# Kernel tuning notes

Hardware: AMD Instinct MI355X
Metric: run time of the kernel (lower is better)

Reference implementation:

```python
import jax, jax.numpy as jnp
import numpy as np

ALPHA = 0.3
TEMPERATURE = 2.0
LN_EPS = 1e-5
NORM_EPS = 1e-8


def setup_inputs() -> dict:
    key = jax.random.key(0)
    k1, k2 = jax.random.split(key)
    B, N, D = 2, 4096, 512
    F = D // 2 + 1  # rfft output bins = 257
    x = jax.random.normal(k1, (B, N, D), dtype=jnp.float32)
    # spectral_proj: Linear(F, F, bias=False); kaiming-uniform-ish scale
    W_spec = jax.random.normal(k2, (F, F), dtype=jnp.float32) * (1.0 / np.sqrt(F))
    gamma = jnp.ones((D,), dtype=jnp.float32)   # LayerNorm weight
    beta = jnp.zeros((D,), dtype=jnp.float32)   # LayerNorm bias
    return {"x": x, "W_spec": W_spec, "gamma": gamma, "beta": beta}


def reference(x, W_spec, gamma, beta):
    # x: (B, N, D) real
    x_hat = jnp.fft.rfft(x, axis=-1)                       # (B, N, F) complex64
    # complex input through real-weight linear: x_hat @ W^T
    x_hat = jnp.einsum('bnf,gf->bng', x_hat, W_spec.astype(x_hat.dtype))
    # complex magnitude normalization per token
    norms = jnp.sqrt(jnp.sum(jnp.abs(x_hat) ** 2, axis=-1, keepdims=True) + NORM_EPS)
    x_norm = x_hat / norms                                 # (B, N, F) complex
    # spectral correlation: |x_norm @ x_norm^H|
    S = jnp.abs(jnp.einsum('bnf,bmf->bnm', x_norm, jnp.conj(x_norm)))  # (B, N, N) real
    S_soft = jax.nn.softmax(S / TEMPERATURE, axis=-1)      # dropout is identity (eval)
    mixed = jnp.einsum('bnm,bmd->bnd', S_soft, x)          # (B, N, D)
    h = x + ALPHA * (mixed - x)                            # residual blend
    # LayerNorm over last dim
    mu = jnp.mean(h, axis=-1, keepdims=True)
    var = jnp.mean((h - mu) ** 2, axis=-1, keepdims=True)
    out = (h - mu) / jnp.sqrt(var + LN_EPS) * gamma + beta
    return out, S
```

## Files before the change

### kernel.cpp

```cpp
#include <hip/hip_runtime.h>
#include <hip/hip_bf16.h>
#include <math.h>

#define BB 2
#define NN 4096
#define DD 512
#define FF 257
#define FP 288
#define KK2 (2*FP)
#define NT 528
#define PI_F 3.14159265358979323846f

typedef __attribute__((ext_vector_type(4))) float f32x4;
typedef __attribute__((ext_vector_type(8))) short bf16x8;
typedef unsigned int u32;
typedef unsigned short u16;

#define MT_OFF  0u
#define XF_OFF  1052672u
#define SS_OFF  10489856u
#define NR_OFF  (SS_OFF + 8388608u)
#define XT_OFF  77598720u
#define MX_OFF  85987328u

#define AS1 __attribute__((address_space(1)))
#define AS3 __attribute__((address_space(3)))

static __device__ __forceinline__ void gl2lds(const u16* g, u16* l) {
    __builtin_amdgcn_global_load_lds((const AS1 u32*)(unsigned long long)g,
                                     (AS3 u32*)(unsigned)(unsigned long long)l,
                                     16, 0, 0);
}

static __device__ __forceinline__ unsigned short f2bf(float f) {
    unsigned int u = __float_as_uint(f);
    unsigned int r = (u + 0x7fffu + ((u >> 16) & 1u)) >> 16;
    return (unsigned short)r;
}
static __device__ __forceinline__ float bf2f(unsigned short s) {
    return __uint_as_float(((unsigned int)s) << 16);
}

static __device__ __forceinline__ bf16x8 conj_swap(bf16x8 a) {
    union { bf16x8 v; u32 u[4]; } s, d;
    s.v = a;
#pragma unroll
    for (int i = 0; i < 4; ++i) {
        u32 w = s.u[i];
        d.u[i] = ((w >> 16) | (w << 16)) ^ 0x80000000u;
    }
    return d.v;
}

__global__ __launch_bounds__(256) void k_zero(float* __restrict__ norms,
                                              u16* __restrict__ Mt) {
    int i = blockIdx.x * 256 + threadIdx.x;
    if (i < 8192) norms[i] = 0.f;
    Mt[514 * 512 + i] = 0;
}

__global__ __launch_bounds__(512) void k_build_Mt(const float* __restrict__ W,
                                                  u16* __restrict__ Mt) {
    __shared__ float twr[512], twi[512], wrow[FF];
    const int g = blockIdx.x;
    const int d = threadIdx.x;
    {
        float s, c;
        sincosf(-(2.0f * PI_F / 512.0f) * (float)d, &s, &c);
        twr[d] = c; twi[d] = s;
    }
    for (int f = d; f < FF; f += 512) wrow[f] = W[g * FF + f];
    __syncthreads();
    float re = 0.f, im = 0.f;
    for (int f = 0; f < FF; ++f) {
        float w = wrow[f];
        int k = (f * d) & 511;
        re = fmaf(w, twr[k], re);
        im = fmaf(w, twi[k], im);
    }
    Mt[(size_t)(2 * g) * 512 + d]     = f2bf(re);
    Mt[(size_t)(2 * g + 1) * 512 + d] = f2bf(im);
}

__global__ __launch_bounds__(256) void k_xcast(const float* __restrict__ x,
                                               u16* __restrict__ xb) {
    const size_t i = ((size_t)blockIdx.x * 256 + threadIdx.x) * 8;
    float4 a = *(const float4*)(x + i);
    float4 b = *(const float4*)(x + i + 4);
    union { u16 h[8]; uint4 q; } o;
    o.h[0] = f2bf(a.x); o.h[1] = f2bf(a.y); o.h[2] = f2bf(a.z); o.h[3] = f2bf(a.w);
    o.h[4] = f2bf(b.x); o.h[5] = f2bf(b.y); o.h[6] = f2bf(b.z); o.h[7] = f2bf(b.w);
    *(uint4*)(xb + i) = o.q;
}

__global__ __launch_bounds__(256) void k_proj_mfma(const u16* __restrict__ xb,
                                                   const u16* __restrict__ Mt,
                                                   u16* __restrict__ xhat,
                                                   float* __restrict__ norms) {
    __shared__ u16 As[128 * 64];
    __shared__ u16 Bs[64 * 64];
    const int prow = blockIdx.y * 128;
    const int gcol = blockIdx.x * 64;
    const int tid = threadIdx.x;
    const int lane = tid & 63;
    const int wave = tid >> 6;
    const int wr = wave * 32;
    const int fr = lane & 15;
    const int q  = lane >> 4;
    const int sw = lane & 7;

    const u16* __restrict__ Arow = xb + (size_t)prow * DD;
    const u16* __restrict__ Brow = Mt + (size_t)gcol * DD;

    const int cs0 = (q ^ sw) * 8;
    const int cs1 = ((4 + q) ^ sw) * 8;

    f32x4 acc[2][4];
#pragma unroll
    for (int m = 0; m < 2; ++m)
#pragma unroll
        for (int n = 0; n < 4; ++n) acc[m][n] = (f32x4)0.f;

    int rA[2], rB[4];
#pragma unroll
    for (int m = 0; m < 2; ++m) rA[m] = (wr + m * 16 + fr) * 64;
#pragma unroll
    for (int n = 0; n < 4; ++n) rB[n] = (n * 16 + fr) * 64;

    for (int kc = 0; kc < DD / 64; ++kc) {
        const int k0 = kc * 64;
        __syncthreads();
#pragma unroll
        for (int it = 0; it < 4; ++it) {
            int e = tid + it * 256;
            int row = e >> 3, ch = e & 7;
            gl2lds(Arow + (size_t)row * DD + k0 + (ch ^ (row & 7)) * 8, &As[e * 8]);
        }
#pragma unroll
        for (int it = 0; it < 2; ++it) {
            int e = tid + it * 256;
            int row = e >> 3, ch = e & 7;
            gl2lds(Brow + (size_t)row * DD + k0 + (ch ^ (row & 7)) * 8, &Bs[e * 8]);
        }
        __syncthreads();
#pragma unroll
        for (int kk = 0; kk < 2; ++kk) {
            const int cs = kk ? cs1 : cs0;
            bf16x8 av[2], bv[4];
#pragma unroll
            for (int m = 0; m < 2; ++m) av[m] = *(const bf16x8*)&As[rA[m] + cs];
#pragma unroll
            for (int n = 0; n < 4; ++n) bv[n] = *(const bf16x8*)&Bs[rB[n] + cs];
#pragma unroll
            for (int m = 0; m < 2; ++m)
#pragma unroll
                for (int n = 0; n < 4; ++n)
                    acc[m][n] = __builtin_amdgcn_mfma_f32_16x16x32_bf16(av[m], bv[n], acc[m][n], 0, 0, 0);
        }
    }

#pragma unroll
    for (int m = 0; m < 2; ++m) {
#pragma unroll
        for (int reg = 0; reg < 4; ++reg) {
            const int r = prow + wr + m * 16 + q * 4 + reg;
            u16* __restrict__ rp = xhat + (size_t)r * KK2 + gcol + fr;
            float sq = 0.f;
#pragma unroll
            for (int n = 0; n < 4; ++n) {
                float v = acc[m][n][reg];
                rp[n * 16] = f2bf(v);
                sq = fmaf(v, v, sq);
            }
            sq += __shfl_xor(sq, 1);
            sq += __shfl_xor(sq, 2);
            sq += __shfl_xor(sq, 4);
            sq += __shfl_xor(sq, 8);
            if (fr == 0) atomicAdd(&norms[r], sq);
        }
    }
}

__global__ __launch_bounds__(256) void k_normalize(u32* __restrict__ Xf,
                                                   const float* __restrict__ norms) {
    const int row = blockIdx.x * 8 + (threadIdx.x >> 5);
    const int l = threadIdx.x & 31;
    const float rn = rsqrtf(norms[row] + 1e-8f);
    u32* __restrict__ p = Xf + (size_t)row * FP;
#pragma unroll
    for (int u = 0; u < 9; ++u) {
        u32 w = p[u * 32 + l];
        float lo = bf2f((u16)(w & 0xffffu)) * rn;
        float hi = bf2f((u16)(w >> 16)) * rn;
        p[u * 32 + l] = (u32)f2bf(lo) | ((u32)f2bf(hi) << 16);
    }
}

__global__ __launch_bounds__(256) void k_gram_mfma(const u16* __restrict__ Xf,
                                                   float* __restrict__ Sout) {
    __shared__ u16 Af[128 * 64];
    __shared__ u16 Bf[128 * 64];
    __shared__ float trs[32][129];
    int i = (int)blockIdx.x;
    int b = 0;
    if (i >= NT) { b = 1; i -= NT; }
    int a = 0;
    while (i >= 32 - a) { i -= 32 - a; ++a; }
    const int brow = a * 128;
    const int bcol = (a + i) * 128;

    const int tid = threadIdx.x;
    const int lane = tid & 63;
    const int wave = tid >> 6;
    const int wr = (wave >> 1) * 64;
    const int wc = (wave & 1) * 64;
    const int fr = lane & 15;
    const int q  = lane >> 4;
    const int sw = lane & 7;

    const u16* __restrict__ Arow = Xf + (size_t)(b * NN + brow) * KK2;
    const u16* __restrict__ Brow = Xf + (size_t)(b * NN + bcol) * KK2;

    int srow[4], soff[4];
#pragma unroll
    for (int it = 0; it < 4; ++it) {
        int e = tid + it * 256;
        int row = e >> 3, ch = e & 7;
        srow[it] = row;
        soff[it] = (ch ^ (row & 7)) * 8;
    }
    const int cs0 = (q ^ sw) * 8;
    const int cs1 = ((4 + q) ^ sw) * 8;

    f32x4 acc_re[4][4], acc_im[4][4];
#pragma unroll
    for (int m = 0; m < 4; ++m)
#pragma unroll
        for (int n = 0; n < 4; ++n) {
            acc_re[m][n] = (f32x4)0.f;
            acc_im[m][n] = (f32x4)0.f;
        }

    int rA[4], rB[4];
#pragma unroll
    for (int m = 0; m < 4; ++m) rA[m] = (wr + m * 16 + fr) * 64;
#pragma unroll
    for (int n = 0; n < 4; ++n) rB[n] = (wc + n * 16 + fr) * 64;

    for (int kc = 0; kc < KK2 / 64; ++kc) {
        const int k0 = kc * 64;
        __syncthreads();
#pragma unroll
        for (int it = 0; it < 4; ++it) {
            int e = tid + it * 256;
            gl2lds(Arow + (size_t)srow[it] * KK2 + k0 + soff[it], &Af[e * 8]);
            gl2lds(Brow + (size_t)srow[it] * KK2 + k0 + soff[it], &Bf[e * 8]);
        }
        __syncthreads();
#pragma unroll
        for (int kk = 0; kk < 2; ++kk) {
            const int cs = kk ? cs1 : cs0;
            bf16x8 av[4], bv[4], gv[4];
#pragma unroll
            for (int m = 0; m < 4; ++m) av[m] = *(const bf16x8*)&Af[rA[m] + cs];
#pragma unroll
            for (int n = 0; n < 4; ++n) bv[n] = *(const bf16x8*)&Bf[rB[n] + cs];
#pragma unroll
            for (int m = 0; m < 4; ++m) gv[m] = conj_swap(av[m]);
#pragma unroll
            for (int m = 0; m < 4; ++m)
#pragma unroll
                for (int n = 0; n < 4; ++n) {
                    acc_re[m][n] = __builtin_amdgcn_mfma_f32_16x16x32_bf16(av[m], bv[n], acc_re[m][n], 0, 0, 0);
                    acc_im[m][n] = __builtin_amdgcn_mfma_f32_16x16x32_bf16(gv[m], bv[n], acc_im[m][n], 0, 0, 0);
                }
        }
    }

    float* __restrict__ Sb = Sout + (size_t)b * NN * NN;
#pragma unroll
    for (int m = 0; m < 4; ++m) {
#pragma unroll
        for (int reg = 0; reg < 4; ++reg) {
            int r = brow + wr + m * 16 + q * 4 + reg;
            float* __restrict__ rp = Sb + (size_t)r * NN + bcol + wc + fr;
#pragma unroll
            for (int n = 0; n < 4; ++n) {
                float re = acc_re[m][n][reg], im = acc_im[m][n][reg];
                rp[n * 16] = sqrtf(fmaf(re, re, im * im));
            }
        }
    }
    if (brow == bcol) return;

#pragma unroll
    for (int p = 0; p < 4; ++p) {
        __syncthreads();
        if ((wave >> 1) == (p >> 1)) {
            const int mbase = (p & 1) * 2;
#pragma unroll
            for (int mm = 0; mm < 2; ++mm) {
                const int m = mbase + mm;
                const int i0 = mm * 16 + q * 4;
#pragma unroll
                for (int reg = 0; reg < 4; ++reg) {
#pragma unroll
                    for (int n = 0; n < 4; ++n) {
                        float re = acc_re[m][n][reg], im = acc_im[m][n][reg];
                        trs[i0 + reg][wc + n * 16 + fr] = sqrtf(fmaf(re, re, im * im));
                    }
                }
            }
        }
        __syncthreads();
        const int j0 = (tid & 7) * 4;
#pragma unroll
        for (int u = 0; u < 4; ++u) {
            const int mr = u * 32 + (tid >> 3);
            float4 v;
            v.x = trs[j0 + 0][mr];
            v.y = trs[j0 + 1][mr];
            v.z = trs[j0 + 2][mr];
            v.w = trs[j0 + 3][mr];
            *(float4*)(Sb + (size_t)(bcol + mr) * NN + brow + p * 32 + j0) = v;
        }
    }
}

__global__ __launch_bounds__(256) void k_softmax(const float* __restrict__ S,
                                                 unsigned short* __restrict__ Wout) {
    __shared__ float red[8];
    const size_t row = blockIdx.x;
    const int tid = threadIdx.x;
    const float4* __restrict__ p4 = (const float4*)(S + row * NN);
    float4 v[4];
    float vmax = -1e30f;
#pragma unroll
    for (int u = 0; u < 4; ++u) {
        v[u] = p4[u * 256 + tid];
        vmax = fmaxf(vmax, fmaxf(fmaxf(v[u].x, v[u].y), fmaxf(v[u].z, v[u].w)));
    }
    for (int off = 32; off > 0; off >>= 1) vmax = fmaxf(vmax, __shfl_down(vmax, off, 64));
    if ((tid & 63) == 0) red[tid >> 6] = vmax;
    __syncthreads();
    const float bmax = fmaxf(fmaxf(red[0], red[1]), fmaxf(red[2], red[3]));
    float s = 0.f;
#pragma unroll
    for (int u = 0; u < 4; ++u) {
        v[u].x = __expf((v[u].x - bmax) * 0.5f);
        v[u].y = __expf((v[u].y - bmax) * 0.5f);
        v[u].z = __expf((v[u].z - bmax) * 0.5f);
        v[u].w = __expf((v[u].w - bmax) * 0.5f);
        s += (v[u].x + v[u].y) + (v[u].z + v[u].w);
    }
    for (int off = 32; off > 0; off >>= 1) s += __shfl_down(s, off, 64);
    if ((tid & 63) == 0) red[4 + (tid >> 6)] = s;
    __syncthreads();
    const float rinv = 1.0f / ((red[4] + red[5]) + (red[6] + red[7]));
    ushort4* __restrict__ o4 = (ushort4*)(Wout + row * NN);
#pragma unroll
    for (int u = 0; u < 4; ++u) {
        ushort4 w;
        w.x = f2bf(v[u].x * rinv);
        w.y = f2bf(v[u].y * rinv);
        w.z = f2bf(v[u].z * rinv);
        w.w = f2bf(v[u].w * rinv);
        o4[u * 256 + tid] = w;
    }
}

__global__ __launch_bounds__(256) void k_xpose(const float* __restrict__ x,
                                               u16* __restrict__ xbT) {
    __shared__ u16 st[64][72];
    const int b = blockIdx.z;
    const int t0 = blockIdx.x * 64;
    const int d0 = blockIdx.y * 64;
    const int tid = threadIdx.x;
#pragma unroll
    for (int u = 0; u < 4; ++u) {
        int idx = tid + u * 256;
        int tl = idx >> 4, d4 = (idx & 15) * 4;
        float4 v = *(const float4*)(x + ((size_t)(b * NN) + t0 + tl) * DD + d0 + d4);
        st[tl][d4 + 0] = f2bf(v.x);
        st[tl][d4 + 1] = f2bf(v.y);
        st[tl][d4 + 2] = f2bf(v.z);
        st[tl][d4 + 3] = f2bf(v.w);
    }
    __syncthreads();
#pragma unroll
    for (int u = 0; u < 2; ++u) {
        int e = tid + u * 256;
        int dl = e >> 3, t8 = (e & 7) * 8;
        union { u16 h[8]; uint4 q; } o;
#pragma unroll
        for (int j = 0; j < 8; ++j) o.h[j] = st[t8 + j][dl];
        *(uint4*)(xbT + ((size_t)(b * DD) + d0 + dl) * NN + t0 + t8) = o.q;
    }
}

__global__ __launch_bounds__(256) void k_mixed_mfma(const u16* __restrict__ Ws,
                                                    const u16* __restrict__ xbT,
                                                    float* __restrict__ mixed) {
    __shared__ u16 As[64 * 64];
    __shared__ u16 Bs[128 * 64];
    const int b = blockIdx.z;
    const int brow = blockIdx.y * 64;
    const int bcol = blockIdx.x * 128;
    const int tid = threadIdx.x;
    const int lane = tid & 63;
    const int wave = tid >> 6;
    const int wr = (wave >> 1) * 32;
    const int wc = (wave & 1) * 64;
    const int fr = lane & 15;
    const int q  = lane >> 4;
    const int sw = lane & 7;

    const u16* __restrict__ Arow = Ws + (size_t)(b * NN + brow) * NN;
    const u16* __restrict__ Brow = xbT + ((size_t)(b * DD) + bcol) * NN;

    const int cs0 = (q ^ sw) * 8;
    const int cs1 = ((4 + q) ^ sw) * 8;

    f32x4 acc[2][4];
#pragma unroll
    for (int m = 0; m < 2; ++m)
#pragma unroll
        for (int n = 0; n < 4; ++n) acc[m][n] = (f32x4)0.f;

    int rA[2], rB[4];
#pragma unroll
    for (int m = 0; m < 2; ++m) rA[m] = (wr + m * 16 + fr) * 64;
#pragma unroll
    for (int n = 0; n < 4; ++n) rB[n] = (wc + n * 16 + fr) * 64;

    for (int kc = 0; kc < NN / 64; ++kc) {
        const int k0 = kc * 64;
        __syncthreads();
#pragma unroll
        for (int it = 0; it < 2; ++it) {
            int e = tid + it * 256;
            int row = e >> 3, ch = e & 7;
            gl2lds(Arow + (size_t)row * NN + k0 + (ch ^ (row & 7)) * 8, &As[e * 8]);
        }
#pragma unroll
        for (int it = 0; it < 4; ++it) {
            int e = tid + it * 256;
            int row = e >> 3, ch = e & 7;
            gl2lds(Brow + (size_t)row * NN + k0 + (ch ^ (row & 7)) * 8, &Bs[e * 8]);
        }
        __syncthreads();
#pragma unroll
        for (int kk = 0; kk < 2; ++kk) {
            const int cs = kk ? cs1 : cs0;
            bf16x8 av[2], bv[4];
#pragma unroll
            for (int m = 0; m < 2; ++m) av[m] = *(const bf16x8*)&As[rA[m] + cs];
#pragma unroll
            for (int n = 0; n < 4; ++n) bv[n] = *(const bf16x8*)&Bs[rB[n] + cs];
#pragma unroll
            for (int m = 0; m < 2; ++m)
#pragma unroll
                for (int n = 0; n < 4; ++n)
                    acc[m][n] = __builtin_amdgcn_mfma_f32_16x16x32_bf16(av[m], bv[n], acc[m][n], 0, 0, 0);
        }
    }

    float* __restrict__ ob = mixed + (size_t)b * NN * DD;
#pragma unroll
    for (int m = 0; m < 2; ++m) {
#pragma unroll
        for (int reg = 0; reg < 4; ++reg) {
            int r = brow + wr + m * 16 + q * 4 + reg;
            float* __restrict__ rp = ob + (size_t)r * DD + bcol + wc + fr;
#pragma unroll
            for (int n = 0; n < 4; ++n) rp[n * 16] = acc[m][n][reg];
        }
    }
}

__global__ __launch_bounds__(256) void k_ln(const float* __restrict__ x,
                                            const float* __restrict__ mixed,
                                            const float* __restrict__ gamma,
                                            const float* __restrict__ beta,
                                            float* __restrict__ out) {
    __shared__ float red[8];
    const size_t row = blockIdx.x;
    const int tid = threadIdx.x;
    const float* __restrict__ xr = x + row * DD;
    const float* __restrict__ mr = mixed + row * DD;
    float x0 = xr[tid], x1 = xr[tid + 256];
    float h0 = fmaf(0.3f, mr[tid] - x0, x0);
    float h1 = fmaf(0.3f, mr[tid + 256] - x1, x1);
    float s = h0 + h1;
    float sq = fmaf(h0, h0, h1 * h1);
    for (int off = 32; off > 0; off >>= 1) {
        s += __shfl_down(s, off, 64);
        sq += __shfl_down(sq, off, 64);
    }
    if ((tid & 63) == 0) { red[tid >> 6] = s; red[4 + (tid >> 6)] = sq; }
    __syncthreads();
    const float mu = ((red[0] + red[1]) + (red[2] + red[3])) * (1.0f / DD);
    const float var = ((red[4] + red[5]) + (red[6] + red[7])) * (1.0f / DD) - mu * mu;
    const float rstd = rsqrtf(var + 1e-5f);
    out[row * DD + tid] = fmaf((h0 - mu) * rstd, gamma[tid], beta[tid]);
    out[row * DD + tid + 256] = fmaf((h1 - mu) * rstd, gamma[tid + 256], beta[tid + 256]);
}

extern "C" void kernel_launch(void* const* d_in, const int* in_sizes, int n_in,
                              void* d_out, int out_size, void* d_ws, size_t ws_size,
                              hipStream_t stream) {
    const float* x     = (const float*)d_in[0];
    const float* Wspec = (const float*)d_in[1];
    const float* gamma = (const float*)d_in[2];
    const float* beta  = (const float*)d_in[3];
    float* out  = (float*)d_out;
    float* Sout = out + (size_t)BB * NN * DD;

    char* ws = (char*)d_ws;
    u16*   Mt    = (u16*)(ws + MT_OFF);
    u16*   Xf    = (u16*)(ws + XF_OFF);
    u32*   XfW   = (u32*)(ws + XF_OFF);
    u16*   xb    = (u16*)(ws + SS_OFF);
    float* norms = (float*)(ws + NR_OFF);
    u16*   Ssoft = (u16*)(ws + SS_OFF);
    u16*   xbT   = (u16*)(ws + XT_OFF);
    float* mixed = (float*)(ws + MX_OFF);

    hipLaunchKernelGGL(k_zero, dim3(124), dim3(256), 0, stream, norms, Mt);
    hipLaunchKernelGGL(k_build_Mt, dim3(257), dim3(512), 0, stream, Wspec, Mt);
    hipLaunchKernelGGL(k_xcast, dim3(2048), dim3(256), 0, stream, x, xb);
    hipLaunchKernelGGL(k_proj_mfma, dim3(KK2 / 64, (BB * NN) / 128), dim3(256), 0, stream,
                       xb, Mt, Xf, norms);
    hipLaunchKernelGGL(k_normalize, dim3(BB * NN / 8), dim3(256), 0, stream, XfW, norms);
    hipLaunchKernelGGL(k_gram_mfma, dim3(BB * NT), dim3(256), 0, stream, Xf, Sout);
    hipLaunchKernelGGL(k_softmax, dim3(BB * NN), dim3(256), 0, stream, Sout, Ssoft);
    hipLaunchKernelGGL(k_xpose, dim3(NN / 64, DD / 64, BB), dim3(256), 0, stream, x, xbT);
    hipLaunchKernelGGL(k_mixed_mfma, dim3(DD / 128, NN / 64, BB), dim3(256), 0, stream, Ssoft, xbT, mixed);
    hipLaunchKernelGGL(k_ln, dim3(BB * NN), dim3(256), 0, stream, x, mixed, gamma, beta, out);
}
```

Before: 386.5 us.

## Fuse softmax into gram epilogue and mixing GEMM, fuse LayerNorm into mixing

Drops the separate softmax kernel. The gram kernel's epilogue now accumulates per-row exp sums, with no max subtraction because |S| <= 1, using atomics into a new lsum buffer. The mixing GEMM reads fp32 S directly, exponentiates and casts to bf16 while staging A tiles, then applies normalization, the residual blend and LayerNorm in its epilogue. This removes the bf16 softmax round trip, the mixed buffer and two launches. In exchange the mixing kernel re-reads fp32 S (twice the bytes of bf16), repeats exp work, holds a much larger LDS B tile (64 KB) with 32-row tiles that lower occupancy, and the gram kernel gains atomics.

```diff
diff --git a/kernel.cpp b/kernel.cpp
--- a/kernel.cpp
+++ b/kernel.cpp
@@ -10,6 +10,7 @@
 #define KK2 (2*FP)
 #define NT 528
 #define PI_F 3.14159265358979323846f
+#define CEXP 0.72134752044f
 
 typedef __attribute__((ext_vector_type(4))) float f32x4;
 typedef __attribute__((ext_vector_type(8))) short bf16x8;
@@ -18,10 +19,10 @@
 
 #define MT_OFF  0u
 #define XF_OFF  1052672u
-#define SS_OFF  10489856u
-#define NR_OFF  (SS_OFF + 8388608u)
+#define XB_OFF  10489856u
+#define NR_OFF  (XB_OFF + 8388608u)
+#define L_OFF   (NR_OFF + 32768u)
 #define XT_OFF  77598720u
-#define MX_OFF  85987328u
 
 #define AS1 __attribute__((address_space(1)))
 #define AS3 __attribute__((address_space(3)))
@@ -53,9 +54,10 @@
 }
 
 __global__ __launch_bounds__(256) void k_zero(float* __restrict__ norms,
+                                              float* __restrict__ l,
                                               u16* __restrict__ Mt) {
     int i = blockIdx.x * 256 + threadIdx.x;
-    if (i < 8192) norms[i] = 0.f;
+    if (i < 8192) { norms[i] = 0.f; l[i] = 0.f; }
     Mt[514 * 512 + i] = 0;
 }
 
@@ -197,10 +199,13 @@
 }
 
 __global__ __launch_bounds__(256) void k_gram_mfma(const u16* __restrict__ Xf,
-                                                   float* __restrict__ Sout) {
-    __shared__ u16 Af[128 * 64];
-    __shared__ u16 Bf[128 * 64];
-    __shared__ float trs[32][129];
+                                                   float* __restrict__ Sout,
+                                                   float* __restrict__ lsum) {
+    __shared__ __align__(16) char gsm[32768];
+    u16* Af = (u16*)gsm;
+    u16* Bf = (u16*)(gsm + 16384);
+    float (*trs)[129] = (float (*)[129])gsm;
+
     int i = (int)blockIdx.x;
     int b = 0;
     if (i >= NT) { b = 1; i -= NT; }
@@ -278,17 +283,26 @@
     }
 
     float* __restrict__ Sb = Sout + (size_t)b * NN * NN;
+    float* __restrict__ lb = lsum + (size_t)b * NN;
 #pragma unroll
     for (int m = 0; m < 4; ++m) {
 #pragma unroll
         for (int reg = 0; reg < 4; ++reg) {
             int r = brow + wr + m * 16 + q * 4 + reg;
             float* __restrict__ rp = Sb + (size_t)r * NN + bcol + wc + fr;
+            float psum = 0.f;
 #pragma unroll
             for (int n = 0; n < 4; ++n) {
                 float re = acc_re[m][n][reg], im = acc_im[m][n][reg];
-                rp[n * 16] = sqrtf(fmaf(re, re, im * im));
+                float s = sqrtf(fmaf(re, re, im * im));
+                rp[n * 16] = s;
+                psum += exp2f(s * CEXP);
             }
+            psum += __shfl_xor(psum, 1);
+            psum += __shfl_xor(psum, 2);
+            psum += __shfl_xor(psum, 4);
+            psum += __shfl_xor(psum, 8);
+            if (fr == 0) atomicAdd(&lb[r], psum);
         }
     }
     if (brow == bcol) return;
@@ -323,49 +337,13 @@
             v.z = trs[j0 + 2][mr];
             v.w = trs[j0 + 3][mr];
             *(float4*)(Sb + (size_t)(bcol + mr) * NN + brow + p * 32 + j0) = v;
-        }
-    }
-}
-
-__global__ __launch_bounds__(256) void k_softmax(const float* __restrict__ S,
-                                                 unsigned short* __restrict__ Wout) {
-    __shared__ float red[8];
-    const size_t row = blockIdx.x;
-    const int tid = threadIdx.x;
-    const float4* __restrict__ p4 = (const float4*)(S + row * NN);
-    float4 v[4];
-    float vmax = -1e30f;
-#pragma unroll
-    for (int u = 0; u < 4; ++u) {
-        v[u] = p4[u * 256 + tid];
-        vmax = fmaxf(vmax, fmaxf(fmaxf(v[u].x, v[u].y), fmaxf(v[u].z, v[u].w)));
-    }
-    for (int off = 32; off > 0; off >>= 1) vmax = fmaxf(vmax, __shfl_down(vmax, off, 64));
-    if ((tid & 63) == 0) red[tid >> 6] = vmax;
-    __syncthreads();
-    const float bmax = fmaxf(fmaxf(red[0], red[1]), fmaxf(red[2], red[3]));
-    float s = 0.f;
-#pragma unroll
-    for (int u = 0; u < 4; ++u) {
-        v[u].x = __expf((v[u].x - bmax) * 0.5f);
-        v[u].y = __expf((v[u].y - bmax) * 0.5f);
-        v[u].z = __expf((v[u].z - bmax) * 0.5f);
-        v[u].w = __expf((v[u].w - bmax) * 0.5f);
-        s += (v[u].x + v[u].y) + (v[u].z + v[u].w);
-    }
-    for (int off = 32; off > 0; off >>= 1) s += __shfl_down(s, off, 64);
-    if ((tid & 63) == 0) red[4 + (tid >> 6)] = s;
-    __syncthreads();
-    const float rinv = 1.0f / ((red[4] + red[5]) + (red[6] + red[7]));
-    ushort4* __restrict__ o4 = (ushort4*)(Wout + row * NN);
-#pragma unroll
-    for (int u = 0; u < 4; ++u) {
-        ushort4 w;
-        w.x = f2bf(v[u].x * rinv);
-        w.y = f2bf(v[u].y * rinv);
-        w.z = f2bf(v[u].z * rinv);
-        w.w = f2bf(v[u].w * rinv);
-        o4[u * 256 + tid] = w;
+            float ps = exp2f(v.x * CEXP) + exp2f(v.y * CEXP)
+                     + exp2f(v.z * CEXP) + exp2f(v.w * CEXP);
+            ps += __shfl_xor(ps, 1);
+            ps += __shfl_xor(ps, 2);
+            ps += __shfl_xor(ps, 4);
+            if ((tid & 7) == 0) atomicAdd(&lb[bcol + mr], ps);
+        }
     }
 }
 
@@ -398,112 +376,132 @@
     }
 }
 
-__global__ __launch_bounds__(256) void k_mixed_mfma(const u16* __restrict__ Ws,
-                                                    const u16* __restrict__ xbT,
-                                                    float* __restrict__ mixed) {
-    __shared__ u16 As[64 * 64];
-    __shared__ u16 Bs[128 * 64];
-    const int b = blockIdx.z;
-    const int brow = blockIdx.y * 64;
-    const int bcol = blockIdx.x * 128;
+__global__ __launch_bounds__(256) void k_mixed_fused(const float* __restrict__ S,
+                                                     const float* __restrict__ lsum,
+                                                     const u16* __restrict__ xbT,
+                                                     const float* __restrict__ x,
+                                                     const float* __restrict__ gamma,
+                                                     const float* __restrict__ beta,
+                                                     float* __restrict__ out) {
+    __shared__ __align__(16) u16 Bs[DD * 64];
+    __shared__ __align__(16) u16 As[32 * 64];
+    __shared__ float red[32][8];
+    const int b = blockIdx.y;
+    const int t0 = blockIdx.x * 32;
     const int tid = threadIdx.x;
     const int lane = tid & 63;
     const int wave = tid >> 6;
-    const int wr = (wave >> 1) * 32;
-    const int wc = (wave & 1) * 64;
     const int fr = lane & 15;
     const int q  = lane >> 4;
     const int sw = lane & 7;
-
-    const u16* __restrict__ Arow = Ws + (size_t)(b * NN + brow) * NN;
-    const u16* __restrict__ Brow = xbT + ((size_t)(b * DD) + bcol) * NN;
+    const int dcol = wave * 128;
+
+    const float* __restrict__ Srow = S + ((size_t)b * NN + t0) * NN;
+    const u16* __restrict__ Brow = xbT + (size_t)b * DD * NN;
 
     const int cs0 = (q ^ sw) * 8;
     const int cs1 = ((4 + q) ^ sw) * 8;
 
-    f32x4 acc[2][4];
+    const int ar = tid >> 3;
+    const int ach = tid & 7;
+    const float* __restrict__ aSrc = Srow + (size_t)ar * NN + ach * 8;
+    u16* __restrict__ aDst = As + ar * 64 + (ach ^ (ar & 7)) * 8;
+
+    f32x4 acc[2][8];
 #pragma unroll
     for (int m = 0; m < 2; ++m)
 #pragma unroll
-        for (int n = 0; n < 4; ++n) acc[m][n] = (f32x4)0.f;
-
-    int rA[2], rB[4];
-#pragma unroll
-    for (int m = 0; m < 2; ++m) rA[m] = (wr + m * 16 + fr) * 64;
-#pragma unroll
-    for (int n = 0; n < 4; ++n) rB[n] = (wc + n * 16 + fr) * 64;
+        for (int n = 0; n < 8; ++n) acc[m][n] = (f32x4)0.f;
+
+    int rA[2], rB[8];
+#pragma unroll
+    for (int m = 0; m < 2; ++m) rA[m] = (m * 16 + fr) * 64;
+#pragma unroll
+    for (int n = 0; n < 8; ++n) rB[n] = (dcol + n * 16 + fr) * 64;
 
     for (int kc = 0; kc < NN / 64; ++kc) {
         const int k0 = kc * 64;
         __syncthreads();
 #pragma unroll
-        for (int it = 0; it < 2; ++it) {
-            int e = tid + it * 256;
-            int row = e >> 3, ch = e & 7;
-            gl2lds(Arow + (size_t)row * NN + k0 + (ch ^ (row & 7)) * 8, &As[e * 8]);
-        }
-#pragma unroll
-        for (int it = 0; it < 4; ++it) {
+        for (int it = 0; it < 16; ++it) {
             int e = tid + it * 256;
             int row = e >> 3, ch = e & 7;
             gl2lds(Brow + (size_t)row * NN + k0 + (ch ^ (row & 7)) * 8, &Bs[e * 8]);
         }
+        {
+            float4 a0 = *(const float4*)(aSrc + k0);
+            float4 a1 = *(const float4*)(aSrc + k0 + 4);
+            union { u16 h[8]; uint4 v; } pk;
+            pk.h[0] = f2bf(exp2f(a0.x * CEXP));
+            pk.h[1] = f2bf(exp2f(a0.y * CEXP));
+            pk.h[2] = f2bf(exp2f(a0.z * CEXP));
+            pk.h[3] = f2bf(exp2f(a0.w * CEXP));
+            pk.h[4] = f2bf(exp2f(a1.x * CEXP));
+            pk.h[5] = f2bf(exp2f(a1.y * CEXP));
+            pk.h[6] = f2bf(exp2f(a1.z * CEXP));
+            pk.h[7] = f2bf(exp2f(a1.w * CEXP));
+            *(uint4*)aDst = pk.v;
+        }
         __syncthreads();
 #pragma unroll
         for (int kk = 0; kk < 2; ++kk) {
             const int cs = kk ? cs1 : cs0;
-            bf16x8 av[2], bv[4];
+            bf16x8 av[2], bv[8];
 #pragma unroll
             for (int m = 0; m < 2; ++m) av[m] = *(const bf16x8*)&As[rA[m] + cs];
 #pragma unroll
-            for (int n = 0; n < 4; ++n) bv[n] = *(const bf16x8*)&Bs[rB[n] + cs];
+            for (int n = 0; n < 8; ++n) bv[n] = *(const bf16x8*)&Bs[rB[n] + cs];
 #pragma unroll
             for (int m = 0; m < 2; ++m)
 #pragma unroll
-                for (int n = 0; n < 4; ++n)
+                for (int n = 0; n < 8; ++n)
                     acc[m][n] = __builtin_amdgcn_mfma_f32_16x16x32_bf16(av[m], bv[n], acc[m][n], 0, 0, 0);
         }
     }
 
-    float* __restrict__ ob = mixed + (size_t)b * NN * DD;
+    __syncthreads();
 #pragma unroll
     for (int m = 0; m < 2; ++m) {
 #pragma unroll
         for (int reg = 0; reg < 4; ++reg) {
-            int r = brow + wr + m * 16 + q * 4 + reg;
-            float* __restrict__ rp = ob + (size_t)r * DD + bcol + wc + fr;
-#pragma unroll
-            for (int n = 0; n < 4; ++n) rp[n * 16] = acc[m][n][reg];
-        }
-    }
-}
-
-__global__ __launch_bounds__(256) void k_ln(const float* __restrict__ x,
-                                            const float* __restrict__ mixed,
-                                            const float* __restrict__ gamma,
-                                            const float* __restrict__ beta,
-                                            float* __restrict__ out) {
-    __shared__ float red[8];
-    const size_t row = blockIdx.x;
-    const int tid = threadIdx.x;
-    const float* __restrict__ xr = x + row * DD;
-    const float* __restrict__ mr = mixed + row * DD;
-    float x0 = xr[tid], x1 = xr[tid + 256];
-    float h0 = fmaf(0.3f, mr[tid] - x0, x0);
-    float h1 = fmaf(0.3f, mr[tid + 256] - x1, x1);
-    float s = h0 + h1;
-    float sq = fmaf(h0, h0, h1 * h1);
-    for (int off = 32; off > 0; off >>= 1) {
-        s += __shfl_down(s, off, 64);
-        sq += __shfl_down(sq, off, 64);
-    }
-    if ((tid & 63) == 0) { red[tid >> 6] = s; red[4 + (tid >> 6)] = sq; }
+            const int r = m * 16 + q * 4 + reg;
+            const float rinv = 1.0f / lsum[(size_t)b * NN + t0 + r];
+            const float* __restrict__ xrow = x + ((size_t)b * NN + t0 + r) * DD;
+            float sh = 0.f, sh2 = 0.f;
+#pragma unroll
+            for (int n = 0; n < 8; ++n) {
+                float xv = xrow[dcol + n * 16 + fr];
+                float h = fmaf(0.3f * rinv, acc[m][n][reg], 0.7f * xv);
+                acc[m][n][reg] = h;
+                sh += h;
+                sh2 = fmaf(h, h, sh2);
+            }
+            sh += __shfl_xor(sh, 1);  sh2 += __shfl_xor(sh2, 1);
+            sh += __shfl_xor(sh, 2);  sh2 += __shfl_xor(sh2, 2);
+            sh += __shfl_xor(sh, 4);  sh2 += __shfl_xor(sh2, 4);
+            sh += __shfl_xor(sh, 8);  sh2 += __shfl_xor(sh2, 8);
+            if (fr == 0) { red[r][wave * 2] = sh; red[r][wave * 2 + 1] = sh2; }
+        }
+    }
     __syncthreads();
-    const float mu = ((red[0] + red[1]) + (red[2] + red[3])) * (1.0f / DD);
-    const float var = ((red[4] + red[5]) + (red[6] + red[7])) * (1.0f / DD) - mu * mu;
-    const float rstd = rsqrtf(var + 1e-5f);
-    out[row * DD + tid] = fmaf((h0 - mu) * rstd, gamma[tid], beta[tid]);
-    out[row * DD + tid + 256] = fmaf((h1 - mu) * rstd, gamma[tid + 256], beta[tid + 256]);
+#pragma unroll
+    for (int m = 0; m < 2; ++m) {
+#pragma unroll
+        for (int reg = 0; reg < 4; ++reg) {
+            const int r = m * 16 + q * 4 + reg;
+            const float s1 = (red[r][0] + red[r][2]) + (red[r][4] + red[r][6]);
+            const float s2 = (red[r][1] + red[r][3]) + (red[r][5] + red[r][7]);
+            const float mu = s1 * (1.0f / DD);
+            const float var = s2 * (1.0f / DD) - mu * mu;
+            const float rstd = rsqrtf(var + 1e-5f);
+            float* __restrict__ orow = out + ((size_t)b * NN + t0 + r) * DD;
+#pragma unroll
+            for (int n = 0; n < 8; ++n) {
+                const int col = dcol + n * 16 + fr;
+                orow[col] = fmaf((acc[m][n][reg] - mu) * rstd, gamma[col], beta[col]);
+            }
+        }
+    }
 }
 
 extern "C" void kernel_launch(void* const* d_in, const int* in_sizes, int n_in,
@@ -520,21 +518,19 @@
     u16*   Mt    = (u16*)(ws + MT_OFF);
     u16*   Xf    = (u16*)(ws + XF_OFF);
     u32*   XfW   = (u32*)(ws + XF_OFF);
-    u16*   xb    = (u16*)(ws + SS_OFF);
+    u16*   xb    = (u16*)(ws + XB_OFF);
     float* norms = (float*)(ws + NR_OFF);
-    u16*   Ssoft = (u16*)(ws + SS_OFF);
+    float* lsum  = (float*)(ws + L_OFF);
     u16*   xbT   = (u16*)(ws + XT_OFF);
-    float* mixed = (float*)(ws + MX_OFF);
-
-    hipLaunchKernelGGL(k_zero, dim3(124), dim3(256), 0, stream, norms, Mt);
+
+    hipLaunchKernelGGL(k_zero, dim3(124), dim3(256), 0, stream, norms, lsum, Mt);
     hipLaunchKernelGGL(k_build_Mt, dim3(257), dim3(512), 0, stream, Wspec, Mt);
     hipLaunchKernelGGL(k_xcast, dim3(2048), dim3(256), 0, stream, x, xb);
     hipLaunchKernelGGL(k_proj_mfma, dim3(KK2 / 64, (BB * NN) / 128), dim3(256), 0, stream,
                        xb, Mt, Xf, norms);
     hipLaunchKernelGGL(k_normalize, dim3(BB * NN / 8), dim3(256), 0, stream, XfW, norms);
-    hipLaunchKernelGGL(k_gram_mfma, dim3(BB * NT), dim3(256), 0, stream, Xf, Sout);
-    hipLaunchKernelGGL(k_softmax, dim3(BB * NN), dim3(256), 0, stream, Sout, Ssoft);
+    hipLaunchKernelGGL(k_gram_mfma, dim3(BB * NT), dim3(256), 0, stream, Xf, Sout, lsum);
     hipLaunchKernelGGL(k_xpose, dim3(NN / 64, DD / 64, BB), dim3(256), 0, stream, x, xbT);
-    hipLaunchKernelGGL(k_mixed_mfma, dim3(DD / 128, NN / 64, BB), dim3(256), 0, stream, Ssoft, xbT, mixed);
-    hipLaunchKernelGGL(k_ln, dim3(BB * NN), dim3(256), 0, stream, x, mixed, gamma, beta, out);
-}
+    hipLaunchKernelGGL(k_mixed_fused, dim3(NN / 32, BB), dim3(256), 0, stream,
+                       Sout, lsum, xbT, x, gamma, beta, out);
+}
```

Result: slower. 440.3 us (+13.9%).
